# Kernel tuning notes

Measured on AMD Instinct MI355X. Metric: run time of the kernel, lower is better.

The kernel has to match this reference:

```python
import jax, jax.numpy as jnp
import numpy as np

EPS = 1e-5
SINKHORN_ITERS = 20
ALPHA_INIT = 0.01


def setup_inputs() -> dict:
    key = jax.random.key(0)
    ks = jax.random.split(key, 8)
    B, n, C = 8192, 4, 2048
    nC = n * C
    return {
        "x_expanded": jax.random.normal(ks[0], (B, n, C), dtype=jnp.float32),
        "rmsnorm_weight": jnp.ones((C,), dtype=jnp.float32),
        "phi_pre": 0.02 * jax.random.normal(ks[1], (n, nC), dtype=jnp.float32),
        "phi_post": 0.02 * jax.random.normal(ks[2], (n, nC), dtype=jnp.float32),
        "phi_res": 0.02 * jax.random.normal(ks[3], (n * n, nC), dtype=jnp.float32),
        "b_pre": jnp.zeros((n,), dtype=jnp.float32),
        "b_post": jnp.zeros((n,), dtype=jnp.float32),
        "b_res": jnp.zeros((n, n), dtype=jnp.float32),
        "alpha_pre": jnp.float32(ALPHA_INIT),
        "alpha_post": jnp.float32(ALPHA_INIT),
        "alpha_res": jnp.float32(ALPHA_INIT),
    }


def _rmsnorm(x, w, eps):
    # RMSNorm over the channel dim C of each stream
    ms = jnp.mean(x * x, axis=-1, keepdims=True)
    return x * jax.lax.rsqrt(ms + eps) * w


def _sinkhorn(logits, iters, eps):
    # logits: (B, n, n) -> doubly-stochastic matrix via Sinkhorn-Knopp
    m = jnp.exp(logits - jnp.max(logits, axis=(1, 2), keepdims=True))
    for _ in range(iters):
        m = m / (jnp.sum(m, axis=2, keepdims=True) + eps)  # row normalize
        m = m / (jnp.sum(m, axis=1, keepdims=True) + eps)  # col normalize
    return m


def reference(x_expanded, rmsnorm_weight, phi_pre, phi_post, phi_res,
              b_pre, b_post, b_res, alpha_pre, alpha_post, alpha_res):
    B, n, C = x_expanded.shape
    x_norm = _rmsnorm(x_expanded, rmsnorm_weight, EPS)   # (B, n, C)
    xf = x_norm.reshape(B, n * C)                         # (B, nC)

    # dynamic mixing coefficients from learned projections
    h_pre = alpha_pre * (xf @ phi_pre.T) + b_pre          # (B, n)
    h_post = alpha_post * (xf @ phi_post.T) + b_post      # (B, n)
    h_res_logits = (alpha_res * (xf @ phi_res.T) + b_res.reshape(-1)).reshape(B, n, n)

    h_res = _sinkhorn(h_res_logits, SINKHORN_ITERS, EPS)  # (B, n, n) doubly stochastic

    # blended mixing of the raw residual streams
    mixed = jnp.einsum('bij,bjc->bic', h_res, x_expanded)        # (B, n, C)
    agg = jnp.einsum('bn,bnc->bc', h_pre, x_expanded)            # (B, C)
    out = mixed + h_post[:, :, None] * agg[:, None, :]           # (B, n, C)
    return out
```

## Files before the change

kernel.cpp:

```cpp
#include <hip/hip_runtime.h>
#include <hip/hip_bf16.h>
#include <cstdint>

#define CH 2048
#define NCF 8192
#define NJ 24
#define RPB 4
#define EPS_F 1e-5f
#define SINK_ITERS 20

typedef float v4f __attribute__((ext_vector_type(4)));

__device__ __forceinline__ uint32_t bf16rne(float f) {
    uint32_t u = __float_as_uint(f);
    return (u + 0x7fffu + ((u >> 16) & 1u)) >> 16;
}

__device__ __forceinline__ float dot8(const uint4& x, const uint4& p, float acc) {
    asm("v_dot2_f32_bf16 %0, %1, %2, %0" : "+v"(acc) : "v"(x.x), "v"(p.x));
    asm("v_dot2_f32_bf16 %0, %1, %2, %0" : "+v"(acc) : "v"(x.y), "v"(p.y));
    asm("v_dot2_f32_bf16 %0, %1, %2, %0" : "+v"(acc) : "v"(x.z), "v"(p.z));
    asm("v_dot2_f32_bf16 %0, %1, %2, %0" : "+v"(acc) : "v"(x.w), "v"(p.w));
    return acc;
}

__global__ void __launch_bounds__(256) prep_phi_kernel(
    const float* __restrict__ w,
    const float* __restrict__ phi_pre,
    const float* __restrict__ phi_post,
    const float* __restrict__ phi_res,
    const float* __restrict__ alpha_pre,
    const float* __restrict__ alpha_post,
    const float* __restrict__ alpha_res,
    uint16_t* __restrict__ phiW)
{
    int idx = blockIdx.x * 256 + threadIdx.x;
    if (idx >= NJ * NCF) return;
    int j = idx / NCF;
    int k = idx - j * NCF;
    int c = k & (CH - 1);
    float v, a;
    if (j < 4)      { v = phi_pre[j * NCF + k];        a = alpha_pre[0]; }
    else if (j < 8) { v = phi_post[(j - 4) * NCF + k]; a = alpha_post[0]; }
    else            { v = phi_res[(j - 8) * NCF + k];  a = alpha_res[0]; }
    phiW[idx] = (uint16_t)bf16rne(v * a * w[c]);
}

__global__ void __launch_bounds__(512) mhc_main_kernel(
    const float* __restrict__ x,
    const uint16_t* __restrict__ phiW,
    const float* __restrict__ b_pre,
    const float* __restrict__ b_post,
    const float* __restrict__ b_res,
    float* __restrict__ out)
{
    const int t = threadIdx.x;
    const int lane = t & 63;
    const int wave = t >> 6;
    const long b0 = (long)blockIdx.x * RPB;

    __shared__ uint32_t xn[RPB][NCF / 2];
    __shared__ float4 red[RPB][8];
    __shared__ float H[RPB][24];

    {
        const float4* xp = reinterpret_cast<const float4*>(x + b0 * NCF);
        #pragma unroll
        for (int r = 0; r < RPB; ++r) {
            float ss0, ss1, ss2, ss3;
            {
                float4 a0 = xp[r * 2048 + t];
                float4 a1 = xp[r * 2048 + t + 512];
                float4 a2 = xp[r * 2048 + t + 1024];
                float4 a3 = xp[r * 2048 + t + 1536];
                ss0 = a0.x*a0.x + a0.y*a0.y + a0.z*a0.z + a0.w*a0.w;
                ss1 = a1.x*a1.x + a1.y*a1.y + a1.z*a1.z + a1.w*a1.w;
                ss2 = a2.x*a2.x + a2.y*a2.y + a2.z*a2.z + a2.w*a2.w;
                ss3 = a3.x*a3.x + a3.y*a3.y + a3.z*a3.z + a3.w*a3.w;
                *reinterpret_cast<uint2*>(&xn[r][2*t]) =
                    make_uint2(bf16rne(a0.x) | (bf16rne(a0.y) << 16),
                               bf16rne(a0.z) | (bf16rne(a0.w) << 16));
                *reinterpret_cast<uint2*>(&xn[r][2*t + 1024]) =
                    make_uint2(bf16rne(a1.x) | (bf16rne(a1.y) << 16),
                               bf16rne(a1.z) | (bf16rne(a1.w) << 16));
                *reinterpret_cast<uint2*>(&xn[r][2*t + 2048]) =
                    make_uint2(bf16rne(a2.x) | (bf16rne(a2.y) << 16),
                               bf16rne(a2.z) | (bf16rne(a2.w) << 16));
                *reinterpret_cast<uint2*>(&xn[r][2*t + 3072]) =
                    make_uint2(bf16rne(a3.x) | (bf16rne(a3.y) << 16),
                               bf16rne(a3.z) | (bf16rne(a3.w) << 16));
            }
            #pragma unroll
            for (int m = 1; m < 64; m <<= 1) {
                ss0 += __shfl_xor(ss0, m, 64);
                ss1 += __shfl_xor(ss1, m, 64);
                ss2 += __shfl_xor(ss2, m, 64);
                ss3 += __shfl_xor(ss3, m, 64);
            }
            if (lane == 0) red[r][wave] = make_float4(ss0, ss1, ss2, ss3);
        }
    }
    __syncthreads();

    float scl[RPB][4];
    #pragma unroll
    for (int r = 0; r < RPB; ++r) {
        float sx = 0.f, sy = 0.f, sz = 0.f, sw = 0.f;
        #pragma unroll
        for (int w8 = 0; w8 < 8; ++w8) {
            float4 v = red[r][w8];
            sx += v.x; sy += v.y; sz += v.z; sw += v.w;
        }
        scl[r][0] = rsqrtf(sx * (1.0f / CH) + EPS_F);
        scl[r][1] = rsqrtf(sy * (1.0f / CH) + EPS_F);
        scl[r][2] = rsqrtf(sz * (1.0f / CH) + EPS_F);
        scl[r][3] = rsqrtf(sw * (1.0f / CH) + EPS_F);
    }

    float accT[3][RPB] = {};
    float accS[3][RPB] = {};
    {
        const uint16_t* pw = phiW + (size_t)(wave * 3) * NCF;
        const int kl = 8 * lane;
        const uint4* xr0 = reinterpret_cast<const uint4*>(xn[0]);
        const uint4* xr1 = reinterpret_cast<const uint4*>(xn[1]);
        const uint4* xr2 = reinterpret_cast<const uint4*>(xn[2]);
        const uint4* xr3 = reinterpret_cast<const uint4*>(xn[3]);

        uint4 pA0 = *reinterpret_cast<const uint4*>(pw + 0 * NCF + kl);
        uint4 pA1 = *reinterpret_cast<const uint4*>(pw + 1 * NCF + kl);
        uint4 pA2 = *reinterpret_cast<const uint4*>(pw + 2 * NCF + kl);
        uint4 xA0 = xr0[lane], xA1 = xr1[lane], xA2 = xr2[lane], xA3 = xr3[lane];

        #pragma unroll
        for (int u = 0; u < 16; u += 2) {
            const int iB = 64 * (u + 1) + lane;
            const int kB = 512 * (u + 1) + kl;
            uint4 pB0 = *reinterpret_cast<const uint4*>(pw + 0 * NCF + kB);
            uint4 pB1 = *reinterpret_cast<const uint4*>(pw + 1 * NCF + kB);
            uint4 pB2 = *reinterpret_cast<const uint4*>(pw + 2 * NCF + kB);
            uint4 xB0 = xr0[iB], xB1 = xr1[iB], xB2 = xr2[iB], xB3 = xr3[iB];

            accS[0][0] = dot8(xA0, pA0, accS[0][0]);
            accS[0][1] = dot8(xA1, pA0, accS[0][1]);
            accS[0][2] = dot8(xA2, pA0, accS[0][2]);
            accS[0][3] = dot8(xA3, pA0, accS[0][3]);
            accS[1][0] = dot8(xA0, pA1, accS[1][0]);
            accS[1][1] = dot8(xA1, pA1, accS[1][1]);
            accS[1][2] = dot8(xA2, pA1, accS[1][2]);
            accS[1][3] = dot8(xA3, pA1, accS[1][3]);
            accS[2][0] = dot8(xA0, pA2, accS[2][0]);
            accS[2][1] = dot8(xA1, pA2, accS[2][1]);
            accS[2][2] = dot8(xA2, pA2, accS[2][2]);
            accS[2][3] = dot8(xA3, pA2, accS[2][3]);

            if (u + 2 < 16) {
                const int iA = 64 * (u + 2) + lane;
                const int kA = 512 * (u + 2) + kl;
                pA0 = *reinterpret_cast<const uint4*>(pw + 0 * NCF + kA);
                pA1 = *reinterpret_cast<const uint4*>(pw + 1 * NCF + kA);
                pA2 = *reinterpret_cast<const uint4*>(pw + 2 * NCF + kA);
                xA0 = xr0[iA]; xA1 = xr1[iA]; xA2 = xr2[iA]; xA3 = xr3[iA];
            }

            accS[0][0] = dot8(xB0, pB0, accS[0][0]);
            accS[0][1] = dot8(xB1, pB0, accS[0][1]);
            accS[0][2] = dot8(xB2, pB0, accS[0][2]);
            accS[0][3] = dot8(xB3, pB0, accS[0][3]);
            accS[1][0] = dot8(xB0, pB1, accS[1][0]);
            accS[1][1] = dot8(xB1, pB1, accS[1][1]);
            accS[1][2] = dot8(xB2, pB1, accS[1][2]);
            accS[1][3] = dot8(xB3, pB1, accS[1][3]);
            accS[2][0] = dot8(xB0, pB2, accS[2][0]);
            accS[2][1] = dot8(xB1, pB2, accS[2][1]);
            accS[2][2] = dot8(xB2, pB2, accS[2][2]);
            accS[2][3] = dot8(xB3, pB2, accS[2][3]);

            if (((u + 1) & 3) == 3) {
                const int s = (u + 1) >> 2;
                #pragma unroll
                for (int jl = 0; jl < 3; ++jl) {
                    #pragma unroll
                    for (int r = 0; r < RPB; ++r) {
                        accT[jl][r] = fmaf(scl[r][s], accS[jl][r], accT[jl][r]);
                        accS[jl][r] = 0.f;
                    }
                }
            }
        }
    }
    {
        #pragma unroll
        for (int m = 1; m < 64; m <<= 1) {
            #pragma unroll
            for (int jl = 0; jl < 3; ++jl) {
                #pragma unroll
                for (int r = 0; r < RPB; ++r)
                    accT[jl][r] += __shfl_xor(accT[jl][r], m, 64);
            }
        }
        if (lane == 0) {
            #pragma unroll
            for (int jl = 0; jl < 3; ++jl) {
                int j = 3 * wave + jl;
                float bias;
                if (j < 4)      bias = b_pre[j];
                else if (j < 8) bias = b_post[j - 4];
                else            bias = b_res[j - 8];
                #pragma unroll
                for (int r = 0; r < RPB; ++r) H[r][j] = accT[jl][r] + bias;
            }
        }
    }
    __syncthreads();

    float msink;
    {
        const int r = lane >> 4;
        const int q = lane & 15;
        float L = H[r][8 + q];
        float mx = L;
        mx = fmaxf(mx, __shfl_xor(mx, 1, 64));
        mx = fmaxf(mx, __shfl_xor(mx, 2, 64));
        mx = fmaxf(mx, __shfl_xor(mx, 4, 64));
        mx = fmaxf(mx, __shfl_xor(mx, 8, 64));
        float m = __expf(L - mx);
        #pragma unroll
        for (int it = 0; it < SINK_ITERS; ++it) {
            float rs = m + __shfl_xor(m, 1, 64);
            rs += __shfl_xor(rs, 2, 64);
            m = m * __builtin_amdgcn_rcpf(rs + EPS_F);
            float cs = m + __shfl_xor(m, 4, 64);
            cs += __shfl_xor(cs, 8, 64);
            m = m * __builtin_amdgcn_rcpf(cs + EPS_F);
        }
        msink = m;
    }

    #pragma unroll
    for (int r = 0; r < RPB; ++r) {
        float hp[4], hq[4], hrm[4][4];
        #pragma unroll
        for (int i = 0; i < 4; ++i) {
            hp[i] = H[r][i];
            hq[i] = H[r][4 + i];
            #pragma unroll
            for (int j = 0; j < 4; ++j)
                hrm[i][j] = __shfl(msink, 16 * r + 4 * i + j, 64);
        }
        float4 s[4];
        #pragma unroll
        for (int jj = 0; jj < 4; ++jj) {
            uint2 pk = *reinterpret_cast<const uint2*>(&xn[r][2 * t + 1024 * jj]);
            s[jj].x = __uint_as_float(pk.x << 16);
            s[jj].y = __uint_as_float(pk.x & 0xffff0000u);
            s[jj].z = __uint_as_float(pk.y << 16);
            s[jj].w = __uint_as_float(pk.y & 0xffff0000u);
        }
        float ax = hp[0]*s[0].x + hp[1]*s[1].x + hp[2]*s[2].x + hp[3]*s[3].x;
        float ay = hp[0]*s[0].y + hp[1]*s[1].y + hp[2]*s[2].y + hp[3]*s[3].y;
        float az = hp[0]*s[0].z + hp[1]*s[1].z + hp[2]*s[2].z + hp[3]*s[3].z;
        float aw = hp[0]*s[0].w + hp[1]*s[1].w + hp[2]*s[2].w + hp[3]*s[3].w;
        v4f* op = reinterpret_cast<v4f*>(out + (b0 + r) * NCF + 4 * t);
        #pragma unroll
        for (int i = 0; i < 4; ++i) {
            v4f o;
            o.x = hrm[i][0]*s[0].x + hrm[i][1]*s[1].x + hrm[i][2]*s[2].x + hrm[i][3]*s[3].x + hq[i]*ax;
            o.y = hrm[i][0]*s[0].y + hrm[i][1]*s[1].y + hrm[i][2]*s[2].y + hrm[i][3]*s[3].y + hq[i]*ay;
            o.z = hrm[i][0]*s[0].z + hrm[i][1]*s[1].z + hrm[i][2]*s[2].z + hrm[i][3]*s[3].z + hq[i]*az;
            o.w = hrm[i][0]*s[0].w + hrm[i][1]*s[1].w + hrm[i][2]*s[2].w + hrm[i][3]*s[3].w + hq[i]*aw;
            __builtin_nontemporal_store(o, op + i * 512);
        }
    }
}

extern "C" void kernel_launch(void* const* d_in, const int* in_sizes, int n_in,
                              void* d_out, int out_size, void* d_ws, size_t ws_size,
                              hipStream_t stream)
{
    const float* x        = (const float*)d_in[0];
    const float* w        = (const float*)d_in[1];
    const float* phi_pre  = (const float*)d_in[2];
    const float* phi_post = (const float*)d_in[3];
    const float* phi_res  = (const float*)d_in[4];
    const float* b_pre    = (const float*)d_in[5];
    const float* b_post   = (const float*)d_in[6];
    const float* b_res    = (const float*)d_in[7];
    const float* a_pre    = (const float*)d_in[8];
    const float* a_post   = (const float*)d_in[9];
    const float* a_res    = (const float*)d_in[10];
    float* out = (float*)d_out;
    uint16_t* phiW = (uint16_t*)d_ws;

    const int B = in_sizes[0] / NCF;

    prep_phi_kernel<<<(NJ * NCF + 255) / 256, 256, 0, stream>>>(
        w, phi_pre, phi_post, phi_res, a_pre, a_post, a_res, phiW);

    mhc_main_kernel<<<B / RPB, 512, 0, stream>>>(
        x, phiW, b_pre, b_post, b_res, out);
}
```

Before: 133.9 us.

## Double block size to 1024 threads, splitting K across wave pairs

Blocks now launch 1024 threads instead of 512. Each thread loads two float4 per row instead of four. Each projection group is split across two waves that each cover half of the K range, with partial sums combined through a new shared-memory reduction step and an extra barrier. The output stage assigns two rows per half-block. The goal is more in-flight memory parallelism and shorter per-thread dependency chains, at the cost of an extra __syncthreads and the launch_bounds(1024,2) register cap.

```diff
diff --git a/kernel.cpp b/kernel.cpp
--- a/kernel.cpp
+++ b/kernel.cpp
@@ -46,7 +46,7 @@
     phiW[idx] = (uint16_t)bf16rne(v * a * w[c]);
 }
 
-__global__ void __launch_bounds__(512) mhc_main_kernel(
+__global__ void __launch_bounds__(1024, 2) mhc_main_kernel(
     const float* __restrict__ x,
     const uint16_t* __restrict__ phiW,
     const float* __restrict__ b_pre,
@@ -60,44 +60,41 @@
     const long b0 = (long)blockIdx.x * RPB;
 
     __shared__ uint32_t xn[RPB][NCF / 2];
-    __shared__ float4 red[RPB][8];
+    __shared__ float redA[RPB][16];
+    __shared__ float redB[RPB][16];
+    __shared__ float hredp[16][12];
     __shared__ float H[RPB][24];
 
     {
         const float4* xp = reinterpret_cast<const float4*>(x + b0 * NCF);
+        float ssA[RPB], ssB[RPB];
         #pragma unroll
         for (int r = 0; r < RPB; ++r) {
-            float ss0, ss1, ss2, ss3;
-            {
-                float4 a0 = xp[r * 2048 + t];
-                float4 a1 = xp[r * 2048 + t + 512];
-                float4 a2 = xp[r * 2048 + t + 1024];
-                float4 a3 = xp[r * 2048 + t + 1536];
-                ss0 = a0.x*a0.x + a0.y*a0.y + a0.z*a0.z + a0.w*a0.w;
-                ss1 = a1.x*a1.x + a1.y*a1.y + a1.z*a1.z + a1.w*a1.w;
-                ss2 = a2.x*a2.x + a2.y*a2.y + a2.z*a2.z + a2.w*a2.w;
-                ss3 = a3.x*a3.x + a3.y*a3.y + a3.z*a3.z + a3.w*a3.w;
-                *reinterpret_cast<uint2*>(&xn[r][2*t]) =
-                    make_uint2(bf16rne(a0.x) | (bf16rne(a0.y) << 16),
-                               bf16rne(a0.z) | (bf16rne(a0.w) << 16));
-                *reinterpret_cast<uint2*>(&xn[r][2*t + 1024]) =
-                    make_uint2(bf16rne(a1.x) | (bf16rne(a1.y) << 16),
-                               bf16rne(a1.z) | (bf16rne(a1.w) << 16));
-                *reinterpret_cast<uint2*>(&xn[r][2*t + 2048]) =
-                    make_uint2(bf16rne(a2.x) | (bf16rne(a2.y) << 16),
-                               bf16rne(a2.z) | (bf16rne(a2.w) << 16));
-                *reinterpret_cast<uint2*>(&xn[r][2*t + 3072]) =
-                    make_uint2(bf16rne(a3.x) | (bf16rne(a3.y) << 16),
-                               bf16rne(a3.z) | (bf16rne(a3.w) << 16));
-            }
-            #pragma unroll
-            for (int m = 1; m < 64; m <<= 1) {
-                ss0 += __shfl_xor(ss0, m, 64);
-                ss1 += __shfl_xor(ss1, m, 64);
-                ss2 += __shfl_xor(ss2, m, 64);
-                ss3 += __shfl_xor(ss3, m, 64);
-            }
-            if (lane == 0) red[r][wave] = make_float4(ss0, ss1, ss2, ss3);
+            float4 a = xp[r * 2048 + t];
+            float4 b = xp[r * 2048 + t + 1024];
+            ssA[r] = a.x*a.x + a.y*a.y + a.z*a.z + a.w*a.w;
+            ssB[r] = b.x*b.x + b.y*b.y + b.z*b.z + b.w*b.w;
+            *reinterpret_cast<uint2*>(&xn[r][2 * t]) =
+                make_uint2(bf16rne(a.x) | (bf16rne(a.y) << 16),
+                           bf16rne(a.z) | (bf16rne(a.w) << 16));
+            *reinterpret_cast<uint2*>(&xn[r][2 * t + 2048]) =
+                make_uint2(bf16rne(b.x) | (bf16rne(b.y) << 16),
+                           bf16rne(b.z) | (bf16rne(b.w) << 16));
+        }
+        #pragma unroll
+        for (int m = 1; m < 64; m <<= 1) {
+            #pragma unroll
+            for (int r = 0; r < RPB; ++r) {
+                ssA[r] += __shfl_xor(ssA[r], m, 64);
+                ssB[r] += __shfl_xor(ssB[r], m, 64);
+            }
+        }
+        if (lane == 0) {
+            #pragma unroll
+            for (int r = 0; r < RPB; ++r) {
+                redA[r][wave] = ssA[r];
+                redB[r][wave] = ssB[r];
+            }
         }
     }
     __syncthreads();
@@ -105,35 +102,43 @@
     float scl[RPB][4];
     #pragma unroll
     for (int r = 0; r < RPB; ++r) {
-        float sx = 0.f, sy = 0.f, sz = 0.f, sw = 0.f;
-        #pragma unroll
-        for (int w8 = 0; w8 < 8; ++w8) {
-            float4 v = red[r][w8];
-            sx += v.x; sy += v.y; sz += v.z; sw += v.w;
-        }
-        scl[r][0] = rsqrtf(sx * (1.0f / CH) + EPS_F);
-        scl[r][1] = rsqrtf(sy * (1.0f / CH) + EPS_F);
-        scl[r][2] = rsqrtf(sz * (1.0f / CH) + EPS_F);
-        scl[r][3] = rsqrtf(sw * (1.0f / CH) + EPS_F);
+        const float4* ra = reinterpret_cast<const float4*>(redA[r]);
+        const float4* rb = reinterpret_cast<const float4*>(redB[r]);
+        float4 a0 = ra[0], a1 = ra[1], a2 = ra[2], a3 = ra[3];
+        float4 c0 = rb[0], c1 = rb[1], c2 = rb[2], c3 = rb[3];
+        float s0 = a0.x+a0.y+a0.z+a0.w + a1.x+a1.y+a1.z+a1.w;
+        float s1 = a2.x+a2.y+a2.z+a2.w + a3.x+a3.y+a3.z+a3.w;
+        float s2 = c0.x+c0.y+c0.z+c0.w + c1.x+c1.y+c1.z+c1.w;
+        float s3 = c2.x+c2.y+c2.z+c2.w + c3.x+c3.y+c3.z+c3.w;
+        scl[r][0] = rsqrtf(s0 * (1.0f / CH) + EPS_F);
+        scl[r][1] = rsqrtf(s1 * (1.0f / CH) + EPS_F);
+        scl[r][2] = rsqrtf(s2 * (1.0f / CH) + EPS_F);
+        scl[r][3] = rsqrtf(s3 * (1.0f / CH) + EPS_F);
     }
 
     float accT[3][RPB] = {};
     float accS[3][RPB] = {};
     {
-        const uint16_t* pw = phiW + (size_t)(wave * 3) * NCF;
+        const int jt = wave >> 1;
+        const int h  = wave & 1;
+        const int u0 = 8 * h;
+        const uint16_t* pw = phiW + (size_t)(jt * 3) * NCF;
         const int kl = 8 * lane;
         const uint4* xr0 = reinterpret_cast<const uint4*>(xn[0]);
         const uint4* xr1 = reinterpret_cast<const uint4*>(xn[1]);
         const uint4* xr2 = reinterpret_cast<const uint4*>(xn[2]);
         const uint4* xr3 = reinterpret_cast<const uint4*>(xn[3]);
 
-        uint4 pA0 = *reinterpret_cast<const uint4*>(pw + 0 * NCF + kl);
-        uint4 pA1 = *reinterpret_cast<const uint4*>(pw + 1 * NCF + kl);
-        uint4 pA2 = *reinterpret_cast<const uint4*>(pw + 2 * NCF + kl);
-        uint4 xA0 = xr0[lane], xA1 = xr1[lane], xA2 = xr2[lane], xA3 = xr3[lane];
-
-        #pragma unroll
-        for (int u = 0; u < 16; u += 2) {
+        const int kF = 512 * u0 + kl;
+        const int iF = 64 * u0 + lane;
+        uint4 pA0 = *reinterpret_cast<const uint4*>(pw + 0 * NCF + kF);
+        uint4 pA1 = *reinterpret_cast<const uint4*>(pw + 1 * NCF + kF);
+        uint4 pA2 = *reinterpret_cast<const uint4*>(pw + 2 * NCF + kF);
+        uint4 xA0 = xr0[iF], xA1 = xr1[iF], xA2 = xr2[iF], xA3 = xr3[iF];
+
+        #pragma unroll
+        for (int du = 0; du < 8; du += 2) {
+            const int u = u0 + du;
             const int iB = 64 * (u + 1) + lane;
             const int kB = 512 * (u + 1) + kl;
             uint4 pB0 = *reinterpret_cast<const uint4*>(pw + 0 * NCF + kB);
@@ -154,7 +159,7 @@
             accS[2][2] = dot8(xA2, pA2, accS[2][2]);
             accS[2][3] = dot8(xA3, pA2, accS[2][3]);
 
-            if (u + 2 < 16) {
+            if (du + 2 < 8) {
                 const int iA = 64 * (u + 2) + lane;
                 const int kA = 512 * (u + 2) + kl;
                 pA0 = *reinterpret_cast<const uint4*>(pw + 0 * NCF + kA);
@@ -201,16 +206,24 @@
         }
         if (lane == 0) {
             #pragma unroll
-            for (int jl = 0; jl < 3; ++jl) {
-                int j = 3 * wave + jl;
-                float bias;
-                if (j < 4)      bias = b_pre[j];
-                else if (j < 8) bias = b_post[j - 4];
-                else            bias = b_res[j - 8];
+            for (int jl = 0; jl < 3; ++jl)
                 #pragma unroll
-                for (int r = 0; r < RPB; ++r) H[r][j] = accT[jl][r] + bias;
-            }
-        }
+                for (int r = 0; r < RPB; ++r)
+                    hredp[wave][jl * 4 + r] = accT[jl][r];
+        }
+    }
+    __syncthreads();
+
+    if (t < 96) {
+        const int j = t >> 2;
+        const int r = t & 3;
+        const int jt2 = j / 3, jl2 = j % 3;
+        float v = hredp[2 * jt2][jl2 * 4 + r] + hredp[2 * jt2 + 1][jl2 * 4 + r];
+        float bias;
+        if (j < 4)      bias = b_pre[j];
+        else if (j < 8) bias = b_post[j - 4];
+        else            bias = b_res[j - 8];
+        H[r][j] = v + bias;
     }
     __syncthreads();
 
@@ -237,39 +250,44 @@
         msink = m;
     }
 
-    #pragma unroll
-    for (int r = 0; r < RPB; ++r) {
-        float hp[4], hq[4], hrm[4][4];
-        #pragma unroll
-        for (int i = 0; i < 4; ++i) {
-            hp[i] = H[r][i];
-            hq[i] = H[r][4 + i];
-            #pragma unroll
-            for (int j = 0; j < 4; ++j)
-                hrm[i][j] = __shfl(msink, 16 * r + 4 * i + j, 64);
-        }
-        float4 s[4];
-        #pragma unroll
-        for (int jj = 0; jj < 4; ++jj) {
-            uint2 pk = *reinterpret_cast<const uint2*>(&xn[r][2 * t + 1024 * jj]);
-            s[jj].x = __uint_as_float(pk.x << 16);
-            s[jj].y = __uint_as_float(pk.x & 0xffff0000u);
-            s[jj].z = __uint_as_float(pk.y << 16);
-            s[jj].w = __uint_as_float(pk.y & 0xffff0000u);
-        }
-        float ax = hp[0]*s[0].x + hp[1]*s[1].x + hp[2]*s[2].x + hp[3]*s[3].x;
-        float ay = hp[0]*s[0].y + hp[1]*s[1].y + hp[2]*s[2].y + hp[3]*s[3].y;
-        float az = hp[0]*s[0].z + hp[1]*s[1].z + hp[2]*s[2].z + hp[3]*s[3].z;
-        float aw = hp[0]*s[0].w + hp[1]*s[1].w + hp[2]*s[2].w + hp[3]*s[3].w;
-        v4f* op = reinterpret_cast<v4f*>(out + (b0 + r) * NCF + 4 * t);
-        #pragma unroll
-        for (int i = 0; i < 4; ++i) {
-            v4f o;
-            o.x = hrm[i][0]*s[0].x + hrm[i][1]*s[1].x + hrm[i][2]*s[2].x + hrm[i][3]*s[3].x + hq[i]*ax;
-            o.y = hrm[i][0]*s[0].y + hrm[i][1]*s[1].y + hrm[i][2]*s[2].y + hrm[i][3]*s[3].y + hq[i]*ay;
-            o.z = hrm[i][0]*s[0].z + hrm[i][1]*s[1].z + hrm[i][2]*s[2].z + hrm[i][3]*s[3].z + hq[i]*az;
-            o.w = hrm[i][0]*s[0].w + hrm[i][1]*s[1].w + hrm[i][2]*s[2].w + hrm[i][3]*s[3].w + hq[i]*aw;
-            __builtin_nontemporal_store(o, op + i * 512);
+    {
+        const int hi = t >> 9;
+        const int q  = t & 511;
+        #pragma unroll
+        for (int rr = 0; rr < 2; ++rr) {
+            const int r = 2 * hi + rr;
+            float hp[4], hq[4], hrm[4][4];
+            #pragma unroll
+            for (int i = 0; i < 4; ++i) {
+                hp[i] = H[r][i];
+                hq[i] = H[r][4 + i];
+                #pragma unroll
+                for (int j = 0; j < 4; ++j)
+                    hrm[i][j] = __shfl(msink, 16 * r + 4 * i + j, 64);
+            }
+            float4 s[4];
+            #pragma unroll
+            for (int jj = 0; jj < 4; ++jj) {
+                uint2 pk = *reinterpret_cast<const uint2*>(&xn[r][2 * q + 1024 * jj]);
+                s[jj].x = __uint_as_float(pk.x << 16);
+                s[jj].y = __uint_as_float(pk.x & 0xffff0000u);
+                s[jj].z = __uint_as_float(pk.y << 16);
+                s[jj].w = __uint_as_float(pk.y & 0xffff0000u);
+            }
+            float ax = hp[0]*s[0].x + hp[1]*s[1].x + hp[2]*s[2].x + hp[3]*s[3].x;
+            float ay = hp[0]*s[0].y + hp[1]*s[1].y + hp[2]*s[2].y + hp[3]*s[3].y;
+            float az = hp[0]*s[0].z + hp[1]*s[1].z + hp[2]*s[2].z + hp[3]*s[3].z;
+            float aw = hp[0]*s[0].w + hp[1]*s[1].w + hp[2]*s[2].w + hp[3]*s[3].w;
+            v4f* op = reinterpret_cast<v4f*>(out + (b0 + r) * NCF + 4 * q);
+            #pragma unroll
+            for (int i = 0; i < 4; ++i) {
+                v4f o;
+                o.x = hrm[i][0]*s[0].x + hrm[i][1]*s[1].x + hrm[i][2]*s[2].x + hrm[i][3]*s[3].x + hq[i]*ax;
+                o.y = hrm[i][0]*s[0].y + hrm[i][1]*s[1].y + hrm[i][2]*s[2].y + hrm[i][3]*s[3].y + hq[i]*ay;
+                o.z = hrm[i][0]*s[0].z + hrm[i][1]*s[1].z + hrm[i][2]*s[2].z + hrm[i][3]*s[3].z + hq[i]*az;
+                o.w = hrm[i][0]*s[0].w + hrm[i][1]*s[1].w + hrm[i][2]*s[2].w + hrm[i][3]*s[3].w + hq[i]*aw;
+                __builtin_nontemporal_store(o, op + i * 512);
+            }
         }
     }
 }
@@ -297,6 +315,6 @@
     prep_phi_kernel<<<(NJ * NCF + 255) / 256, 256, 0, stream>>>(
         w, phi_pre, phi_post, phi_res, a_pre, a_post, a_res, phiW);
 
-    mhc_main_kernel<<<B / RPB, 512, 0, stream>>>(
+    mhc_main_kernel<<<B / RPB, 1024, 0, stream>>>(
         x, phiW, b_pre, b_post, b_res, out);
 }
```

Result: slower. 203.5 us (+52.0%).
